# Optimization experiments

Measured on AMD Instinct MI355X. Metric: run time of the kernel, lower is better.

## Reference

```python
import jax, jax.numpy as jnp
import numpy as np

WIN_SIZE = 16
STRIDE = 8
H = W = 512
B = 8
C = 3


def gaussian_blend(win_size):
    # matches WindowOverlapProcessor._create_gaussian_weights
    sigma = win_size / 4.0
    x = jnp.arange(win_size, dtype=jnp.float32) - (win_size - 1) / 2.0
    g = jnp.exp(-(x ** 2) / (2.0 * sigma ** 2))
    g = g / g.sum()
    return g[:, None] * g[None, :]  # [ws, ws]


def setup_inputs() -> dict:
    key = jax.random.key(0)
    hw = (H - WIN_SIZE) // STRIDE + 1  # 63
    ww = (W - WIN_SIZE) // STRIDE + 1  # 63
    nw = hw * ww  # 3969
    hs = (jnp.arange(hw) * STRIDE).astype(jnp.int64 if jax.config.jax_enable_x64 else jnp.int32)
    ws_ = (jnp.arange(ww) * STRIDE).astype(hs.dtype)
    coords = jnp.stack(
        [jnp.repeat(hs, ww), jnp.tile(ws_, hw)], axis=-1
    )  # [nw, 2] regular overlapping grid
    windows = jax.random.normal(key, (B, nw, WIN_SIZE, WIN_SIZE, C), dtype=jnp.float32)
    return {
        "windows": windows,
        "window_coords": coords,
        "h_windows": hw,
        "w_windows": ww,
        "stride": STRIDE,
        "original_h": H,
        "original_w": W,
        "channels": C,
    }


def reference(windows, window_coords, h_windows, w_windows, stride,
              original_h, original_w, channels):
    Bb, nw, ws, _, Cc = windows.shape
    blend = gaussian_blend(ws)  # [ws, ws]

    # flat pixel index for every window element
    dh = jnp.arange(ws)
    dw = jnp.arange(ws)
    offs = dh[:, None] * original_w + dw[None, :]            # [ws, ws]
    base = window_coords[:, 0] * original_w + window_coords[:, 1]  # [nw]
    idx = (base[:, None, None] + offs[None]).reshape(-1)     # [nw*ws*ws]

    # weighted window values, [B, C, nw*ws*ws]
    contrib = windows * blend[None, None, :, :, None]
    contrib = contrib.transpose(0, 4, 1, 2, 3).reshape(Bb, Cc, -1)

    recon = jnp.zeros((Bb, Cc, original_h * original_w), windows.dtype)
    recon = recon.at[:, :, idx].add(contrib)

    wsum = jnp.zeros((original_h * original_w,), blend.dtype)
    wsum = wsum.at[idx].add(jnp.tile(blend.reshape(-1), nw))

    recon = recon / (wsum[None, None, :] + 1e-8)
    return recon.reshape(Bb, Cc, original_h, original_w)
```

## Files before the change

### kernel.cpp

```cpp
#include <hip/hip_runtime.h>


#define OH 512
#define OW 512
#define NB 8
#define NC 3
#define STR 8
#define HWIN 63
#define NWIN (HWIN * HWIN)
#define PLANE (OH * OW)

struct F3 { float x, y, z; };

__device__ __forceinline__ float gblend(int d) {
    const float x = (float)d - 7.5f;
    return __expf(-(x * x) * 0.03125f) * 0.10442840f;
}

__global__ __launch_bounds__(512) void window_overlap_kernel(
    const float* __restrict__ win, float* __restrict__ out) {
    const int w = threadIdx.x;
    const int h = blockIdx.x & (OH - 1);
    const int b = blockIdx.x >> 9;

    const int i1 = min(h >> 3, HWIN - 1);
    const int dh1 = h - i1 * STR;
    const int i0 = max(i1 - 1, 0);
    const int dh0 = (dh1 <= 7) ? dh1 + 8 : dh1;

    const int j1 = min(w >> 3, HWIN - 1);
    const int dw1 = w - j1 * STR;
    const int j0 = max(j1 - 1, 0);
    const int dw0 = (dw1 <= 7) ? dw1 + 8 : dw1;

    const F3* __restrict__ wp = (const F3*)win;
    const int r0 = (b * NWIN + i0 * HWIN) * 256 + dh0 * 16;
    const int r1 = (b * NWIN + i1 * HWIN) * 256 + dh1 * 16;
    const F3 v00 = wp[r0 + j0 * 256 + dw0];
    const F3 v01 = wp[r0 + j1 * 256 + dw1];
    const F3 v10 = wp[r1 + j0 * 256 + dw0];
    const F3 v11 = wp[r1 + j1 * 256 + dw1];

    const float gh1 = gblend(dh1);
    const float gh0 = (i1 >= 1 && dh1 <= 7) ? gblend(dh0) : 0.0f;
    const float gw1 = gblend(dw1);
    const float gw0 = (j1 >= 1 && dw1 <= 7) ? gblend(dw0) : 0.0f;

    const float r = __builtin_amdgcn_rcpf((gh0 + gh1) * (gw0 + gw1) + 1e-8f);

    const float ax = gh0 * (gw0 * v00.x + gw1 * v01.x) + gh1 * (gw0 * v10.x + gw1 * v11.x);
    const float ay = gh0 * (gw0 * v00.y + gw1 * v01.y) + gh1 * (gw0 * v10.y + gw1 * v11.y);
    const float az = gh0 * (gw0 * v00.z + gw1 * v01.z) + gh1 * (gw0 * v10.z + gw1 * v11.z);

    const int p = b * (NC * PLANE) + h * OW + w;
    __builtin_nontemporal_store(ax * r, &out[p]);
    __builtin_nontemporal_store(ay * r, &out[p + PLANE]);
    __builtin_nontemporal_store(az * r, &out[p + 2 * PLANE]);
}

extern "C" void kernel_launch(void* const* d_in, const int* in_sizes, int n_in,
                              void* d_out, int out_size, void* d_ws, size_t ws_size,
                              hipStream_t stream) {
    const float* windows = (const float*)d_in[0];
    float* out = (float*)d_out;
    window_overlap_kernel<<<NB * OH, 512, 0, stream>>>(windows, out);
}
```

Before: 160.6 us.

## Process eight contiguous pixels per thread with vectorized float4 loads and stores

Each thread now reconstructs an 8-pixel horizontal strip, loading whole 8-column half-rows of the four overlapping windows as float4 vectors instead of scattered 12-byte loads per pixel. Horizontal blend weights come from a constant table and outputs are written with 128-bit nontemporal stores. This targets poor load coalescing and per-pixel instruction overhead, at the cost of more registers per thread and fewer threads overall.

Measured after the change: 198.7 us. 23.8% more time.

```diff
diff --git a/kernel.cpp b/kernel.cpp
--- a/kernel.cpp
+++ b/kernel.cpp
@@ -5,57 +5,88 @@
 #define OW 512
 #define NB 8
 #define NC 3
-#define STR 8
 #define HWIN 63
 #define NWIN (HWIN * HWIN)
 #define PLANE (OH * OW)
 
-struct F3 { float x, y, z; };
+typedef float f4 __attribute__((ext_vector_type(4)));
 
 __device__ __forceinline__ float gblend(int d) {
     const float x = (float)d - 7.5f;
-    return __expf(-(x * x) * 0.03125f) * 0.10442840f;
+    return __expf(-(x * x) * 0.03125f) * 0.1044284f;
 }
 
-__global__ __launch_bounds__(512) void window_overlap_kernel(
+__device__ __forceinline__ float getf(const f4 (&a)[6], int f) {
+    return a[f >> 2][f & 3];
+}
+
+__global__ __launch_bounds__(256) void window_overlap_kernel(
     const float* __restrict__ win, float* __restrict__ out) {
-    const int w = threadIdx.x;
-    const int h = blockIdx.x & (OH - 1);
-    const int b = blockIdx.x >> 9;
+    const int g = blockIdx.x * 256 + threadIdx.x;
+    const int j = g & 63;
+    const int h = (g >> 6) & (OH - 1);
+    const int b = g >> 15;
 
     const int i1 = min(h >> 3, HWIN - 1);
-    const int dh1 = h - i1 * STR;
+    const int dh1 = h - i1 * 8;
     const int i0 = max(i1 - 1, 0);
     const int dh0 = (dh1 <= 7) ? dh1 + 8 : dh1;
-
-    const int j1 = min(w >> 3, HWIN - 1);
-    const int dw1 = w - j1 * STR;
-    const int j0 = max(j1 - 1, 0);
-    const int dw0 = (dw1 <= 7) ? dw1 + 8 : dw1;
-
-    const F3* __restrict__ wp = (const F3*)win;
-    const int r0 = (b * NWIN + i0 * HWIN) * 256 + dh0 * 16;
-    const int r1 = (b * NWIN + i1 * HWIN) * 256 + dh1 * 16;
-    const F3 v00 = wp[r0 + j0 * 256 + dw0];
-    const F3 v01 = wp[r0 + j1 * 256 + dw1];
-    const F3 v10 = wp[r1 + j0 * 256 + dw0];
-    const F3 v11 = wp[r1 + j1 * 256 + dw1];
-
     const float gh1 = gblend(dh1);
     const float gh0 = (i1 >= 1 && dh1 <= 7) ? gblend(dh0) : 0.0f;
-    const float gw1 = gblend(dw1);
-    const float gw0 = (j1 >= 1 && dw1 <= 7) ? gblend(dw0) : 0.0f;
 
-    const float r = __builtin_amdgcn_rcpf((gh0 + gh1) * (gw0 + gw1) + 1e-8f);
+    const int jB = min(j, HWIN - 1);
+    const int jA = max(j - 1, 0);
+    const float fA = (j >= 1) ? 1.0f : 0.0f;
+    const float fB = (j <= HWIN - 1) ? 1.0f : 0.0f;
 
-    const float ax = gh0 * (gw0 * v00.x + gw1 * v01.x) + gh1 * (gw0 * v10.x + gw1 * v11.x);
-    const float ay = gh0 * (gw0 * v00.y + gw1 * v01.y) + gh1 * (gw0 * v10.y + gw1 * v11.y);
-    const float az = gh0 * (gw0 * v00.z + gw1 * v01.z) + gh1 * (gw0 * v10.z + gw1 * v11.z);
+    const f4* __restrict__ w4 = (const f4*)win;
+    const int rb = b * NWIN;
+    const int offA = (rb + i0 * HWIN + jA) * 192 + dh0 * 12 + 6;
+    const int offB = (rb + i0 * HWIN + jB) * 192 + dh0 * 12;
+    const int offC = (rb + i1 * HWIN + jA) * 192 + dh1 * 12 + 6;
+    const int offD = (rb + i1 * HWIN + jB) * 192 + dh1 * 12;
 
-    const int p = b * (NC * PLANE) + h * OW + w;
-    __builtin_nontemporal_store(ax * r, &out[p]);
-    __builtin_nontemporal_store(ay * r, &out[p + PLANE]);
-    __builtin_nontemporal_store(az * r, &out[p + 2 * PLANE]);
+    f4 A[6], Bv[6], Cv[6], Dv[6];
+#pragma unroll
+    for (int k = 0; k < 6; ++k) A[k] = w4[offA + k];
+#pragma unroll
+    for (int k = 0; k < 6; ++k) Bv[k] = w4[offB + k];
+#pragma unroll
+    for (int k = 0; k < 6; ++k) Cv[k] = w4[offC + k];
+#pragma unroll
+    for (int k = 0; k < 6; ++k) Dv[k] = w4[offD + k];
+
+    const float GT[16] = {0.0180058f, 0.0278880f, 0.0405766f, 0.0554615f,
+                          0.0712141f, 0.0859006f, 0.0973380f, 0.1036157f,
+                          0.1036157f, 0.0973380f, 0.0859006f, 0.0712141f,
+                          0.0554615f, 0.0405766f, 0.0278880f, 0.0180058f};
+
+    const float ghs = gh0 + gh1;
+    float o[NC][8];
+#pragma unroll
+    for (int c = 0; c < 8; ++c) {
+        const float wAc = fA * GT[c + 8];
+        const float wBc = fB * GT[c];
+        const float r = __builtin_amdgcn_rcpf(ghs * (wAc + wBc) + 1e-8f);
+        const float aA = wAc * gh0, aC = wAc * gh1;
+        const float aB = wBc * gh0, aD = wBc * gh1;
+#pragma unroll
+        for (int ch = 0; ch < NC; ++ch) {
+            const int f = 3 * c + ch;
+            const float v = aA * getf(A, f) + aC * getf(Cv, f) +
+                            aB * getf(Bv, f) + aD * getf(Dv, f);
+            o[ch][c] = v * r;
+        }
+    }
+
+    const int p = b * (NC * PLANE) + h * OW + (j << 3);
+#pragma unroll
+    for (int ch = 0; ch < NC; ++ch) {
+        const f4 lo = {o[ch][0], o[ch][1], o[ch][2], o[ch][3]};
+        const f4 hi = {o[ch][4], o[ch][5], o[ch][6], o[ch][7]};
+        __builtin_nontemporal_store(lo, (f4*)&out[p + ch * PLANE]);
+        __builtin_nontemporal_store(hi, (f4*)&out[p + ch * PLANE + 4]);
+    }
 }
 
 extern "C" void kernel_launch(void* const* d_in, const int* in_sizes, int n_in,
@@ -63,5 +94,5 @@
                               hipStream_t stream) {
     const float* windows = (const float*)d_in[0];
     float* out = (float*)d_out;
-    window_overlap_kernel<<<NB * OH, 512, 0, stream>>>(windows, out);
+    window_overlap_kernel<<<(NB * OH * (OW / 8)) / 256, 256, 0, stream>>>(windows, out);
 }
```
